# Kernel tuning notes

Hardware: AMD Instinct MI355X
Metric: run time of the kernel (lower is better)

The kernel has to match this reference:

```python
import jax, jax.numpy as jnp
import numpy as np

B, DIM_IN, T = 16, 512, 2048
DIM_OUT2 = 512 * 2  # dim_out * 2 (GLU halves it)
K = 3
STYLE = 128
SCALE_CONV = 1.0 / np.sqrt(DIM_IN * K ** 2).astype(np.float32)  # fan_in = dim_in * k^2 (as in source)
SCALE_LIN = 1.0 / np.sqrt(STYLE).astype(np.float32)


def setup_inputs() -> dict:
    key = jax.random.key(0)
    ks = jax.random.split(key, 6)
    x = jax.random.normal(ks[0], (B, DIM_IN, T), dtype=jnp.float32)
    c_src = jax.random.normal(ks[1], (B, STYLE), dtype=jnp.float32)
    c_trg = jax.random.normal(ks[2], (B, STYLE), dtype=jnp.float32)
    # EqualLinear params (lr_mul=1): weight ~ N(0,1), bias filled with bias_init=1
    w_s = jax.random.normal(ks[3], (DIM_IN, STYLE), dtype=jnp.float32)
    b_s = jnp.ones((DIM_IN,), dtype=jnp.float32)
    w_b = jax.random.normal(ks[4], (DIM_IN, STYLE), dtype=jnp.float32)
    b_b = jnp.ones((DIM_IN,), dtype=jnp.float32)
    weight = jax.random.normal(ks[5], (1, DIM_OUT2, DIM_IN, K), dtype=jnp.float32)
    return {"x": x, "c_src": c_src, "c_trg": c_trg,
            "w_s": w_s, "b_s": b_s, "w_b": w_b, "b_b": b_b, "weight": weight}


def reference(x, c_src, c_trg, w_s, b_s, w_b, b_b, weight):
    bsz, cin, t = x.shape
    cout = weight.shape[1]  # dim_out * 2
    k = weight.shape[3]
    # EqualLinear: F.linear(c, w*scale, bias)
    s = (c_trg @ (w_s * SCALE_LIN).T + b_s).reshape(bsz, 1, cin, 1)
    beta = (c_trg @ (w_b * SCALE_LIN).T + b_b).reshape(bsz, 1, cin, 1)
    w = SCALE_CONV * (weight * s + beta)               # [B, Cout, Cin, K]
    demod = jax.lax.rsqrt(jnp.sum(w * w, axis=(2, 3)) + 1e-8)   # [B, Cout]
    demod_mean = jnp.mean(w.reshape(bsz, cout, -1), axis=2)      # [B, Cout]
    w = (w - demod_mean[:, :, None, None]) * demod[:, :, None, None]
    # batch-as-groups conv1d
    w = w.reshape(bsz * cout, cin, k)
    xr = x.reshape(1, bsz * cin, t)
    out = jax.lax.conv_general_dilated(
        xr, w, window_strides=(1,), padding=[(k // 2, k // 2)],
        dimension_numbers=("NCH", "OIH", "NCH"), feature_group_count=bsz)
    out = out.reshape(bsz, cout, -1)
    a, g = jnp.split(out, 2, axis=1)  # GLU on channel dim
    return a * jax.nn.sigmoid(g)
```

## Files before the change

kernel.cpp:

```cpp
#include <hip/hip_runtime.h>
#include <math.h>

typedef __attribute__((ext_vector_type(8))) short short8;
typedef __attribute__((ext_vector_type(8))) unsigned short ushort8;
typedef __attribute__((ext_vector_type(4))) float f32x4;
typedef unsigned short ushortT;

#define NB     16
#define CIN    512
#define TT     2048
#define COUT2  1024
#define NSTYLE 128
#define KKTOT  1536
#define TPAD   2050
#define NKT    24

#define SCALE_LIN  0.088388347648318447f
#define SCALE_CONV 0.014731391274719736f

__device__ __forceinline__ ushortT f2bf(float f) {
  union { float f; unsigned u; } v; v.f = f;
  unsigned r = v.u + 0x7fffu + ((v.u >> 16) & 1u);
  return (ushortT)(r >> 16);
}

__device__ __forceinline__ void gload16(const void* g, void* l) {
  __builtin_amdgcn_global_load_lds(
      (const __attribute__((address_space(1))) void*)g,
      (__attribute__((address_space(3))) void*)l, 16, 0, 0);
}

__global__ void style_kernel(const float* __restrict__ c_trg,
                             const float* __restrict__ w_s, const float* __restrict__ b_s,
                             const float* __restrict__ w_b, const float* __restrict__ b_b,
                             float* __restrict__ s, float* __restrict__ beta,
                             ushortT* __restrict__ xT) {
  int gid = blockIdx.x * 256 + threadIdx.x;
  int b = gid >> 9, ci = gid & 511;
  const float* ct = c_trg + b * NSTYLE;
  const float* ws = w_s + ci * NSTYLE;
  const float* wb = w_b + ci * NSTYLE;
  float as = 0.f, ab = 0.f;
#pragma unroll 8
  for (int j = 0; j < NSTYLE; ++j) {
    float c = ct[j];
    as += c * ws[j];
    ab += c * wb[j];
  }
  s[gid]    = as * SCALE_LIN + b_s[ci];
  beta[gid] = ab * SCALE_LIN + b_b[ci];
  xT[(size_t)b * TPAD * CIN + ci] = 0;
  xT[((size_t)b * TPAD + TPAD - 1) * CIN + ci] = 0;
}

__global__ void xpose_kernel(const float* __restrict__ x, ushortT* __restrict__ xT) {
  int b = blockIdx.z, ct = blockIdx.y, tt = blockIdx.x;
  int t0 = tt * 64, ci0 = ct * 64;
  __shared__ float tile[64][65];
  const float* xB = x + (size_t)b * CIN * TT;
  int rr = threadIdx.x >> 4;
  int c4 = threadIdx.x & 15;
#pragma unroll
  for (int it = 0; it < 4; ++it) {
    int ci = rr + it * 16;
    float4 v = *(const float4*)(xB + (size_t)(ci0 + ci) * TT + t0 + c4 * 4);
    tile[ci][c4 * 4 + 0] = v.x; tile[ci][c4 * 4 + 1] = v.y;
    tile[ci][c4 * 4 + 2] = v.z; tile[ci][c4 * 4 + 3] = v.w;
  }
  __syncthreads();
  ushortT* xTB = xT + (size_t)b * TPAD * CIN;
#pragma unroll
  for (int it = 0; it < 2; ++it) {
    int idx = it * 256 + threadIdx.x;
    int c8 = idx & 7;
    int tl = idx >> 3;
    union { ushort8 v; ushortT u[8]; } o;
#pragma unroll
    for (int j = 0; j < 8; ++j) o.u[j] = f2bf(tile[c8 * 8 + j][tl]);
    *(ushort8*)(xTB + (size_t)(1 + t0 + tl) * CIN + ci0 + c8 * 8) = o.v;
  }
}

__global__ void modw_kernel(const float* __restrict__ weight,
                            const float* __restrict__ s, const float* __restrict__ beta,
                            ushortT* __restrict__ wnorm) {
  int co = blockIdx.x, tid = threadIdx.x;
  int ci = tid * 2;
  const float* wp = weight + (size_t)co * KKTOT + (size_t)ci * 3;
  float2 va = *(const float2*)(wp);
  float2 vb = *(const float2*)(wp + 2);
  float2 vc = *(const float2*)(wp + 4);
  float v0 = va.x, v1 = va.y, v2 = vb.x, v3 = vb.y, v4 = vc.x, v5 = vc.y;
  int r = ((co & 511) << 1) | (co >> 9);
  __shared__ float rs[4], rq[4];
  for (int b = 0; b < NB; ++b) {
    float2 sv = *(const float2*)(s + b * CIN + ci);
    float2 ev = *(const float2*)(beta + b * CIN + ci);
    float w0 = SCALE_CONV * (v0 * sv.x + ev.x);
    float w1 = SCALE_CONV * (v1 * sv.x + ev.x);
    float w2 = SCALE_CONV * (v2 * sv.x + ev.x);
    float w3 = SCALE_CONV * (v3 * sv.y + ev.y);
    float w4 = SCALE_CONV * (v4 * sv.y + ev.y);
    float w5 = SCALE_CONV * (v5 * sv.y + ev.y);
    float sum = w0 + w1 + w2 + w3 + w4 + w5;
    float sq  = w0*w0 + w1*w1 + w2*w2 + w3*w3 + w4*w4 + w5*w5;
#pragma unroll
    for (int off = 32; off; off >>= 1) {
      sum += __shfl_xor(sum, off);
      sq  += __shfl_xor(sq,  off);
    }
    if ((tid & 63) == 0) { rs[tid >> 6] = sum; rq[tid >> 6] = sq; }
    __syncthreads();
    float mean  = (rs[0] + rs[1] + rs[2] + rs[3]) * (1.0f / 1536.0f);
    float demod = rsqrtf(rq[0] + rq[1] + rq[2] + rq[3] + 1e-8f);
    ushortT* dst = wnorm + ((size_t)b * COUT2 + r) * KKTOT;
    ushort2 p0, p1, p2;
    p0.x = f2bf((w0 - mean) * demod); p0.y = f2bf((w3 - mean) * demod);
    p1.x = f2bf((w1 - mean) * demod); p1.y = f2bf((w4 - mean) * demod);
    p2.x = f2bf((w2 - mean) * demod); p2.y = f2bf((w5 - mean) * demod);
    *(ushort2*)(dst +        ci) = p0;
    *(ushort2*)(dst +  512 + ci) = p1;
    *(ushort2*)(dst + 1024 + ci) = p2;
    __syncthreads();
  }
}


#define AFRAG(d, s, f) (*(const short8*)(ldsc + ((d) * 4 + (s)) * 16384 + aoff + (f) * 1024))
#define BFRAG(d, s, g) (*(const short8*)(ldsc + ((d) * 4 + (s)) * 16384 + boff + (g) * 1024))

#define RDA(as_, d, s, mh) do {              \
    as_##0 = AFRAG(d, s, (mh) * 4 + 0);      \
    as_##1 = AFRAG(d, s, (mh) * 4 + 1);      \
    as_##2 = AFRAG(d, s, (mh) * 4 + 2);      \
    as_##3 = AFRAG(d, s, (mh) * 4 + 3);      \
  } while (0)

#define RDB(bs_, d, s) do {                  \
    bs_##0 = BFRAG(d, s, 0);                 \
    bs_##1 = BFRAG(d, s, 1);                 \
    bs_##2 = BFRAG(d, s, 2);                 \
    bs_##3 = BFRAG(d, s, 3);                 \
  } while (0)

#define STAGE_A(d, s, kt) do {                                                   \
    int kc_ = (kt) * 64 + (s) * 32;                                              \
    gload16(wB + (size_t)(co0 + r0) * KKTOT + kc_ + jbs8,                        \
            ldsw + ((d) * 4 + (s)) * 8192 + tid * 8);                            \
    gload16(wB + (size_t)(co0 + r0 + 128) * KKTOT + kc_ + jbs8,                  \
            ldsw + ((d) * 4 + (s)) * 8192 + 4096 + tid * 8);                     \
  } while (0)

#define STAGE_B(d, s, kt) do {                                                   \
    int kc_ = (kt) * 64 + (s) * 32;                                              \
    int tap_ = kc_ >> 9; int ci_ = kc_ & 511;                                    \
    gload16(xB + (size_t)(t0 + r0 + tap_) * CIN + ci_ + jbs8,                    \
            ldsw + ((d) * 4 + 2 + (s)) * 8192 + tid * 8);                        \
    gload16(xB + (size_t)(t0 + r0 + 128 + tap_) * CIN + ci_ + jbs8,              \
            ldsw + ((d) * 4 + 2 + (s)) * 8192 + 4096 + tid * 8);                 \
  } while (0)

#define PHASE(mh, au_, bu_, RD_CODE, STAGES, VMN, BAR) do {                      \
    if (BAR) {                                                                   \
      if ((VMN) == 6)      asm volatile("s_waitcnt vmcnt(6)" ::: "memory");      \
      else if ((VMN) == 4) asm volatile("s_waitcnt vmcnt(4)" ::: "memory");      \
      else if ((VMN) == 0) asm volatile("s_waitcnt vmcnt(0)" ::: "memory");      \
      __builtin_amdgcn_s_barrier();                                              \
    }                                                                            \
    STAGES;                                                                      \
    RD_CODE;                                                                     \
    __builtin_amdgcn_s_setprio(1);                                               \
    acc[(mh)*4+0][0] = __builtin_amdgcn_mfma_f32_16x16x32_bf16(au_##0, bu_##0, acc[(mh)*4+0][0], 0, 0, 0); \
    acc[(mh)*4+0][1] = __builtin_amdgcn_mfma_f32_16x16x32_bf16(au_##0, bu_##1, acc[(mh)*4+0][1], 0, 0, 0); \
    acc[(mh)*4+0][2] = __builtin_amdgcn_mfma_f32_16x16x32_bf16(au_##0, bu_##2, acc[(mh)*4+0][2], 0, 0, 0); \
    acc[(mh)*4+0][3] = __builtin_amdgcn_mfma_f32_16x16x32_bf16(au_##0, bu_##3, acc[(mh)*4+0][3], 0, 0, 0); \
    acc[(mh)*4+1][0] = __builtin_amdgcn_mfma_f32_16x16x32_bf16(au_##1, bu_##0, acc[(mh)*4+1][0], 0, 0, 0); \
    acc[(mh)*4+1][1] = __builtin_amdgcn_mfma_f32_16x16x32_bf16(au_##1, bu_##1, acc[(mh)*4+1][1], 0, 0, 0); \
    acc[(mh)*4+1][2] = __builtin_amdgcn_mfma_f32_16x16x32_bf16(au_##1, bu_##2, acc[(mh)*4+1][2], 0, 0, 0); \
    acc[(mh)*4+1][3] = __builtin_amdgcn_mfma_f32_16x16x32_bf16(au_##1, bu_##3, acc[(mh)*4+1][3], 0, 0, 0); \
    acc[(mh)*4+2][0] = __builtin_amdgcn_mfma_f32_16x16x32_bf16(au_##2, bu_##0, acc[(mh)*4+2][0], 0, 0, 0); \
    acc[(mh)*4+2][1] = __builtin_amdgcn_mfma_f32_16x16x32_bf16(au_##2, bu_##1, acc[(mh)*4+2][1], 0, 0, 0); \
    acc[(mh)*4+2][2] = __builtin_amdgcn_mfma_f32_16x16x32_bf16(au_##2, bu_##2, acc[(mh)*4+2][2], 0, 0, 0); \
    acc[(mh)*4+2][3] = __builtin_amdgcn_mfma_f32_16x16x32_bf16(au_##2, bu_##3, acc[(mh)*4+2][3], 0, 0, 0); \
    acc[(mh)*4+3][0] = __builtin_amdgcn_mfma_f32_16x16x32_bf16(au_##3, bu_##0, acc[(mh)*4+3][0], 0, 0, 0); \
    acc[(mh)*4+3][1] = __builtin_amdgcn_mfma_f32_16x16x32_bf16(au_##3, bu_##1, acc[(mh)*4+3][1], 0, 0, 0); \
    acc[(mh)*4+3][2] = __builtin_amdgcn_mfma_f32_16x16x32_bf16(au_##3, bu_##2, acc[(mh)*4+3][2], 0, 0, 0); \
    acc[(mh)*4+3][3] = __builtin_amdgcn_mfma_f32_16x16x32_bf16(au_##3, bu_##3, acc[(mh)*4+3][3], 0, 0, 0); \
    __builtin_amdgcn_s_setprio(0);                                               \
  } while (0)

__global__ __launch_bounds__(512, 2)
void conv_gemm8(const ushortT* __restrict__ wnorm, const ushortT* __restrict__ xT,
                float* __restrict__ out) {
  extern __shared__ ushortT ldsw[];
  const char* ldsc = (const char*)ldsw;

  int orig = blockIdx.x;
  int wgid = (orig & 7) * 64 + (orig >> 3);
  int b  = wgid >> 5;
  int i5 = wgid & 31;
  int mp = i5 >> 4, r2 = i5 & 15;
  int nt = r2 >> 1, mt = mp * 2 + (r2 & 1);
  int co0 = mt * 256, t0 = nt * 256;

  int tid = threadIdx.x;
  int l = tid & 63, w = tid >> 6;
  int wm = w & 1, wn = w >> 1;

  int r0 = tid >> 2;
  int jbs8 = (((tid & 3) ^ ((r0 >> 1) & 3)) << 3);
  int cb = ((l >> 4) ^ ((l >> 1) & 3));
  int aoff = (wm * 128 + (l & 15)) * 64 + cb * 16;
  int boff = 32768 + (wn * 64 + (l & 15)) * 64 + cb * 16;

  const ushortT* wB = wnorm + (size_t)b * COUT2 * KKTOT;
  const ushortT* xB = xT + (size_t)b * TPAD * CIN;

  f32x4 acc[8][4];
#pragma unroll
  for (int i = 0; i < 8; ++i)
#pragma unroll
    for (int j = 0; j < 4; ++j)
      acc[i][j] = (f32x4){0.f, 0.f, 0.f, 0.f};
  short8 ax0 = {}, ax1 = {}, ax2 = {}, ax3 = {};
  short8 ay0 = {}, ay1 = {}, ay2 = {}, ay3 = {};
  short8 bx0 = {}, bx1 = {}, bx2 = {}, bx3 = {};
  short8 by0 = {}, by1 = {}, by2 = {}, by3 = {};

  STAGE_A(0, 0, 0); STAGE_B(0, 0, 0); STAGE_A(0, 1, 0); STAGE_B(0, 1, 0);
  STAGE_B(1, 0, 1); STAGE_A(1, 0, 1); STAGE_B(1, 1, 1);
  asm volatile("s_waitcnt vmcnt(6)" ::: "memory");
  __builtin_amdgcn_s_barrier();
  RDA(ax, 0, 0, 0);
  RDB(bx, 0, 0);

  for (int j = 0; j < 11; ++j) {
    int kt1 = 2 * j + 1;
    int k0n = 2 * j + 2, k1n = 2 * j + 3;
    PHASE(0, ax, bx, { RDA(ay, 0, 0, 1); },                STAGE_A(1, 1, kt1),  6, 1);
    PHASE(1, ay, bx, { RDA(ax, 0, 1, 0); RDB(by, 0, 1); }, STAGE_B(0, 0, k0n), -1, 0);
    PHASE(0, ax, by, { RDA(ay, 0, 1, 1); },                STAGE_A(0, 0, k0n),  6, 1);
    PHASE(1, ay, by, { RDA(ax, 1, 0, 0); RDB(bx, 1, 0); }, STAGE_B(0, 1, k0n), -1, 0);
    PHASE(0, ax, bx, { RDA(ay, 1, 0, 1); },                STAGE_A(0, 1, k0n),  6, 1);
    PHASE(1, ay, bx, { RDA(ax, 1, 1, 0); RDB(by, 1, 1); }, STAGE_B(1, 0, k1n), -1, 0);
    PHASE(0, ax, by, { RDA(ay, 1, 1, 1); },                STAGE_A(1, 0, k1n),  6, 1);
    PHASE(1, ay, by, { RDA(ax, 0, 0, 0); RDB(bx, 0, 0); }, STAGE_B(1, 1, k1n), -1, 0);
  }
  PHASE(0, ax, bx, { RDA(ay, 0, 0, 1); },                STAGE_A(1, 1, 23),  6, 1);
  PHASE(1, ay, bx, { RDA(ax, 0, 1, 0); RDB(by, 0, 1); }, {},                -1, 0);
  PHASE(0, ax, by, { RDA(ay, 0, 1, 1); },                {},                 4, 1);
  PHASE(1, ay, by, { RDA(ax, 1, 0, 0); RDB(bx, 1, 0); }, {},                -1, 0);
  PHASE(0, ax, bx, { RDA(ay, 1, 0, 1); },                {},                 0, 1);
  PHASE(1, ay, bx, { RDA(ax, 1, 1, 0); RDB(by, 1, 1); }, {},                -1, 0);
  PHASE(0, ax, by, { RDA(ay, 1, 1, 1); },                {},                -1, 1);
  PHASE(1, ay, by, { },                                  {},                -1, 0);

#pragma unroll
  for (int f = 0; f < 8; ++f) {
    int cop = co0 + wm * 128 + f * 16 + ((l >> 4) << 2);
    int c = cop >> 1;
    size_t obase = ((size_t)b * (COUT2 / 2) + c) * TT;
#pragma unroll
    for (int g = 0; g < 4; ++g) {
      int t = t0 + wn * 64 + g * 16 + (l & 15);
      f32x4 v = acc[f][g];
      out[obase + t]      = v.x / (1.f + __expf(-v.y));
      out[obase + TT + t] = v.z / (1.f + __expf(-v.w));
    }
  }
}

extern "C" void kernel_launch(void* const* d_in, const int* in_sizes, int n_in,
                              void* d_out, int out_size, void* d_ws, size_t ws_size,
                              hipStream_t stream) {
  const float* x      = (const float*)d_in[0];
  const float* c_trg  = (const float*)d_in[2];
  const float* w_s    = (const float*)d_in[3];
  const float* b_s    = (const float*)d_in[4];
  const float* w_b    = (const float*)d_in[5];
  const float* b_b    = (const float*)d_in[6];
  const float* weight = (const float*)d_in[7];
  float* out = (float*)d_out;

  char* ws = (char*)d_ws;
  float*   s     = (float*)ws;
  float*   beta  = (float*)(ws + 32768);
  ushortT* xT    = (ushortT*)(ws + 65536);
  ushortT* wnorm = (ushortT*)(ws + 65536 + 33587200);

  (void)hipFuncSetAttribute((const void*)conv_gemm8,
                            hipFuncAttributeMaxDynamicSharedMemorySize, 131072);

  style_kernel<<<32, 256, 0, stream>>>(c_trg, w_s, b_s, w_b, b_b, s, beta, xT);
  xpose_kernel<<<dim3(32, 8, 16), 256, 0, stream>>>(x, xT);
  modw_kernel<<<1024, 256, 0, stream>>>(weight, s, beta, wnorm);
  conv_gemm8<<<512, 512, 131072, stream>>>(wnorm, xT, out);
}
```

Before: 136.3 us.

## Restructure weight modulation to wave-per-batch and add MFMA sched barrier

The weight-modulation kernel now gives each wavefront four batches, and each lane handles 8 input channels times 3 taps. The per-batch reduction stays inside one wave, so the shared-memory exchange and the two block barriers per batch are gone, and stores become 16-byte vectors instead of ushort2. It also inserts a sched_barrier before the MFMA block in the GEMM phase macro, which stops the compiler from interleaving LDS reads with the MFMAs. The cost is higher register use in the modulation kernel and a more constrained instruction schedule in the main kernel.

New measurement: 132.6 us. 1.03x faster.

```diff
diff --git a/kernel.cpp b/kernel.cpp
--- a/kernel.cpp
+++ b/kernel.cpp
@@ -84,44 +84,51 @@
 __global__ void modw_kernel(const float* __restrict__ weight,
                             const float* __restrict__ s, const float* __restrict__ beta,
                             ushortT* __restrict__ wnorm) {
-  int co = blockIdx.x, tid = threadIdx.x;
-  int ci = tid * 2;
-  const float* wp = weight + (size_t)co * KKTOT + (size_t)ci * 3;
-  float2 va = *(const float2*)(wp);
-  float2 vb = *(const float2*)(wp + 2);
-  float2 vc = *(const float2*)(wp + 4);
-  float v0 = va.x, v1 = va.y, v2 = vb.x, v3 = vb.y, v4 = vc.x, v5 = vc.y;
+  int co = blockIdx.x;
+  int wv = threadIdx.x >> 6;
+  int l  = threadIdx.x & 63;
+  const float* wp = weight + (size_t)co * KKTOT + l * 24;
+  float v[24];
+#pragma unroll
+  for (int j = 0; j < 6; ++j) {
+    float4 t = *(const float4*)(wp + j * 4);
+    v[j * 4 + 0] = t.x; v[j * 4 + 1] = t.y; v[j * 4 + 2] = t.z; v[j * 4 + 3] = t.w;
+  }
   int r = ((co & 511) << 1) | (co >> 9);
-  __shared__ float rs[4], rq[4];
-  for (int b = 0; b < NB; ++b) {
-    float2 sv = *(const float2*)(s + b * CIN + ci);
-    float2 ev = *(const float2*)(beta + b * CIN + ci);
-    float w0 = SCALE_CONV * (v0 * sv.x + ev.x);
-    float w1 = SCALE_CONV * (v1 * sv.x + ev.x);
-    float w2 = SCALE_CONV * (v2 * sv.x + ev.x);
-    float w3 = SCALE_CONV * (v3 * sv.y + ev.y);
-    float w4 = SCALE_CONV * (v4 * sv.y + ev.y);
-    float w5 = SCALE_CONV * (v5 * sv.y + ev.y);
-    float sum = w0 + w1 + w2 + w3 + w4 + w5;
-    float sq  = w0*w0 + w1*w1 + w2*w2 + w3*w3 + w4*w4 + w5*w5;
+#pragma unroll
+  for (int bi = 0; bi < 4; ++bi) {
+    int b = wv * 4 + bi;
+    const float* sp = s + b * CIN + l * 8;
+    const float* ep = beta + b * CIN + l * 8;
+    float4 s0 = *(const float4*)(sp), s1 = *(const float4*)(sp + 4);
+    float4 e0 = *(const float4*)(ep), e1 = *(const float4*)(ep + 4);
+    float sv[8] = {s0.x, s0.y, s0.z, s0.w, s1.x, s1.y, s1.z, s1.w};
+    float ev[8] = {e0.x, e0.y, e0.z, e0.w, e1.x, e1.y, e1.z, e1.w};
+    float wm[24];
+    float sum = 0.f, sq = 0.f;
+#pragma unroll
+    for (int c = 0; c < 8; ++c)
+#pragma unroll
+      for (int k = 0; k < 3; ++k) {
+        float val = SCALE_CONV * (v[c * 3 + k] * sv[c] + ev[c]);
+        wm[c * 3 + k] = val;
+        sum += val; sq += val * val;
+      }
 #pragma unroll
     for (int off = 32; off; off >>= 1) {
       sum += __shfl_xor(sum, off);
       sq  += __shfl_xor(sq,  off);
     }
-    if ((tid & 63) == 0) { rs[tid >> 6] = sum; rq[tid >> 6] = sq; }
-    __syncthreads();
-    float mean  = (rs[0] + rs[1] + rs[2] + rs[3]) * (1.0f / 1536.0f);
-    float demod = rsqrtf(rq[0] + rq[1] + rq[2] + rq[3] + 1e-8f);
+    float mean  = sum * (1.0f / 1536.0f);
+    float demod = rsqrtf(sq + 1e-8f);
     ushortT* dst = wnorm + ((size_t)b * COUT2 + r) * KKTOT;
-    ushort2 p0, p1, p2;
-    p0.x = f2bf((w0 - mean) * demod); p0.y = f2bf((w3 - mean) * demod);
-    p1.x = f2bf((w1 - mean) * demod); p1.y = f2bf((w4 - mean) * demod);
-    p2.x = f2bf((w2 - mean) * demod); p2.y = f2bf((w5 - mean) * demod);
-    *(ushort2*)(dst +        ci) = p0;
-    *(ushort2*)(dst +  512 + ci) = p1;
-    *(ushort2*)(dst + 1024 + ci) = p2;
-    __syncthreads();
+#pragma unroll
+    for (int k = 0; k < 3; ++k) {
+      union { ushort8 v8; ushortT u[8]; } o;
+#pragma unroll
+      for (int c = 0; c < 8; ++c) o.u[c] = f2bf((wm[c * 3 + k] - mean) * demod);
+      *(ushort8*)(dst + k * 512 + l * 8) = o.v8;
+    }
   }
 }
 
@@ -169,6 +176,7 @@
     }                                                                            \
     STAGES;                                                                      \
     RD_CODE;                                                                     \
+    __builtin_amdgcn_sched_barrier(0);     \
     __builtin_amdgcn_s_setprio(1);                                               \
     acc[(mh)*4+0][0] = __builtin_amdgcn_mfma_f32_16x16x32_bf16(au_##0, bu_##0, acc[(mh)*4+0][0], 0, 0, 0); \
     acc[(mh)*4+0][1] = __builtin_amdgcn_mfma_f32_16x16x32_bf16(au_##0, bu_##1, acc[(mh)*4+0][1], 0, 0, 0); \
```
